# Performance work log

Hardware: AMD Instinct MI355X
Metric: run time of the kernel (lower is better)

## Reference

```python
import jax, jax.numpy as jnp
import numpy as np

NFFT = 640
HOP = 320
REF_CH = 3  # reference microphone index


def _hann(n):
    # periodic Hann, matches torch.hann_window(n)
    return 0.5 * (1.0 - jnp.cos(2.0 * jnp.pi * jnp.arange(n, dtype=jnp.float32) / n))


def _stft(x):
    # x: [..., T] -> complex [..., F, Tf], center=True, constant (zero) pad
    win = _hann(NFFT)
    pad = NFFT // 2
    xp = jnp.pad(x, [(0, 0)] * (x.ndim - 1) + [(pad, pad)])
    T = x.shape[-1]
    nf = 1 + T // HOP
    idx = jnp.arange(nf)[:, None] * HOP + jnp.arange(NFFT)[None, :]
    frames = xp[..., idx] * win  # [..., Tf, NFFT]
    return jnp.swapaxes(jnp.fft.rfft(frames, axis=-1), -1, -2)  # [..., F, Tf]


def _istft(S):
    # S: [..., F, Tf] complex -> real [..., (Tf-1)*HOP]
    win = _hann(NFFT)
    frames = jnp.fft.irfft(jnp.swapaxes(S, -1, -2), n=NFFT, axis=-1) * win
    Tf = S.shape[-1]
    L = (Tf - 1) * HOP + NFFT
    idx = jnp.arange(Tf)[:, None] * HOP + jnp.arange(NFFT)[None, :]
    out = jnp.zeros(S.shape[:-2] + (L,), frames.dtype).at[..., idx].add(frames)
    wsum = jnp.zeros((L,), frames.dtype).at[idx].add(win * win)
    out = out / jnp.where(wsum > 1e-11, wsum, 1.0)
    p = NFFT // 2
    return out[..., p:L - p]


def _cov_features(xb):
    # xb: [C, T] -> [C*(C+1) + 2, F, Tf]
    S = _stft(xb)  # [C, F, Tf] complex
    C = xb.shape[0]
    iu, ju = np.triu_indices(C)  # upper triangle, row-major (matches torch mask order)
    cov = S[iu] * jnp.conj(S[ju])  # [C*(C+1)/2, F, Tf], cov[i,j] = S_i * conj(S_j)
    nF, nT = S.shape[-2], S.shape[-1]
    cov_ri = jnp.stack([cov.real, cov.imag], axis=1).reshape(-1, nF, nT)  # interleave re/im
    ref = S[REF_CH]
    return jnp.concatenate([cov_ri, ref.real[None], ref.imag[None]], axis=0)


def _forward(x, rtf_g, ref_g):
    B, C, T = x.shape
    feats = jax.vmap(_cov_features)(x)  # [B, 74, F, Tf]
    # STFT of generated reference channel
    refS = _stft(ref_g.reshape(B, -1))  # [B, F, Tf] complex
    nF, nT = refS.shape[-2], refS.shape[-1]
    # deep-filtering: unfold kernel (3,9) with padding (1,4) over (freq, frame)
    rp = jnp.pad(refS, ((0, 0), (1, 1), (4, 4)))
    patches = jnp.stack([rp[:, ki:ki + nF, kj:kj + nT]
                         for ki in range(3) for kj in range(9)], axis=1)  # [B, 27, F, Tf]
    rtf_c = (rtf_g[..., 0] + 1j * rtf_g[..., 1]).reshape(B, C - 1, 27, nF, nT)
    est = jnp.einsum('bmkft,bkft->bmft', rtf_c, patches)  # [B, C-1, F, Tf]
    est_audio = _istft(est.reshape(B * (C - 1), nF, nT)).reshape(B, C - 1, -1)
    valid = min(est_audio.shape[-1], ref_g.shape[-1])
    all_ch = jnp.concatenate([est_audio[:, :REF_CH, :valid],
                              ref_g[..., :valid],
                              est_audio[:, REF_CH:, :valid]], axis=1)  # [B, C, valid]
    return all_ch[0].T, feats


def setup_inputs() -> dict:
    key = jax.random.key(0)
    k1, k2, k3 = jax.random.split(key, 3)
    B, C, T = 2, 8, 96000
    nF, nT = NFFT // 2 + 1, 1 + T // HOP  # 321, 301
    x = jax.random.normal(k1, (B, C, T), dtype=jnp.float32)
    rtf_g = jax.random.normal(k2, (B, C - 1, 3, 9, nF, nT, 2), dtype=jnp.float32) * 0.1
    ref_g = jax.random.normal(k3, (B, 1, T), dtype=jnp.float32)
    return {"x": x, "rtf_g": rtf_g, "ref_g": ref_g}


def reference(x, rtf_g, ref_g):
    return _forward(x, rtf_g, ref_g)
```

## Files before the change

kernel.cpp:

```cpp
#include <hip/hip_runtime.h>
#include <math.h>

#define TLEN 96000
#define NFFT 640
#define HOP  320
#define NF   321
#define NT   301
#define FT   (NF * NT)

#define TWO_PI_F 6.28318530717958647692f

__constant__ int IU[36] = {0,0,0,0,0,0,0,0, 1,1,1,1,1,1,1, 2,2,2,2,2,2,
                           3,3,3,3,3, 4,4,4,4, 5,5,5, 6,6, 7};
__constant__ int JU[36] = {0,1,2,3,4,5,6,7, 1,2,3,4,5,6,7, 2,3,4,5,6,7,
                           3,4,5,6,7, 4,5,6,7, 5,6,7, 6,7, 7};

__global__ __launch_bounds__(192) void k_stft(const float* __restrict__ x,
                                              const float* __restrict__ ref_g,
                                              float2* __restrict__ Sx,
                                              float2* __restrict__ refS) {
    const int f   = blockIdx.x;
    const int s   = blockIdx.y;
    const int tid = threadIdx.x;

    __shared__ __align__(16) float2 ff[320];

    const float* sig = (s < 16) ? (x + (size_t)s * TLEN) : ref_g;
    for (int n = tid; n < 320; n += 192) {
        const int p0 = f * HOP + n - HOP;
        const int p1 = p0 + 320;
        const float c = cosf((TWO_PI_F / NFFT) * (float)n);
        float v0 = (p0 >= 0 && p0 < TLEN) ? sig[p0] : 0.0f;
        float v1 = (p1 < TLEN) ? sig[p1] : 0.0f;
        v0 *= (0.5f - 0.5f * c);
        v1 *= (0.5f + 0.5f * c);
        float2 o; o.x = v0 + v1; o.y = v0 - v1;
        ff[n] = o;
    }
    __syncthreads();

    if (tid < 161) {
        const int ke = 2 * tid;
        const int ko = ke + 1;
        const float we = (TWO_PI_F / NFFT) * (float)ke;
        const float wo = (TWO_PI_F / NFFT) * (float)ko;
        const float c2e = 2.0f * cosf(we);
        const float c2o = 2.0f * cosf(wo);

        float se1 = 0.0f, se2 = 0.0f, so1 = 0.0f, so2 = 0.0f;
#pragma unroll 8
        for (int n = 0; n < 320; ++n) {
            const float2 v = ff[n];
            const float te = fmaf(c2e, se1, v.x - se2); se2 = se1; se1 = te;
            const float to = fmaf(c2o, so1, v.y - so2); so2 = so1; so1 = to;
        }

        float sE, cE; sincosf(we, &sE, &cE);
        float sO, cO; sincosf(wo, &sO, &cO);
        float2 Xe, Xo;
        Xe.x = cE * se1 - se2;
        Xe.y = sE * se1;
        Xo.x = -(cO * so1 - so2);
        Xo.y = -(sO * so1);

        if (s < 16) {
            float2* base = Sx + (size_t)s * FT;
            base[(size_t)ke * NT + f] = Xe;
            if (ko < 320) base[(size_t)ko * NT + f] = Xo;
        } else {
            refS[(size_t)ke * NT + f] = Xe;
            if (ko < 320) refS[(size_t)ko * NT + f] = Xo;
        }
    }
}

__global__ void k_cov(const float2* __restrict__ Sx, float* __restrict__ feats) {
    int idx = blockIdx.x * blockDim.x + threadIdx.x;
    if (idx >= 2 * 37 * FT) return;
    const int kt  = idx % FT;
    const int job = (idx / FT) % 37;
    const int b   = idx / (37 * FT);
    const float2* Sb = Sx + (size_t)b * 8 * FT;
    float* fb = feats + (size_t)b * 74 * FT;
    if (job == 36) {
        const float2 r = Sb[(size_t)3 * FT + kt];
        fb[(size_t)72 * FT + kt] = r.x;
        fb[(size_t)73 * FT + kt] = r.y;
    } else {
        const float2 a = Sb[(size_t)IU[job] * FT + kt];
        const float2 c = Sb[(size_t)JU[job] * FT + kt];
        fb[(size_t)(2 * job)     * FT + kt] = a.x * c.x + a.y * c.y;
        fb[(size_t)(2 * job + 1) * FT + kt] = a.y * c.x - a.x * c.y;
    }
}

__global__ void k_dfilter(const float2* __restrict__ rtf,
                          const float2* __restrict__ refS,
                          float2* __restrict__ est) {
    int idx = blockIdx.x * blockDim.x + threadIdx.x;
    if (idx >= 7 * FT) return;
    const int t = idx % NT;
    const int f = (idx / NT) % NF;
    const int m = idx / FT;
    float er = 0.0f, ei = 0.0f;
#pragma unroll
    for (int ki = 0; ki < 3; ++ki) {
        const int ff = f + ki - 1;
#pragma unroll
        for (int kj = 0; kj < 9; ++kj) {
            const int tt = t + kj - 4;
            float pr = 0.0f, pi = 0.0f;
            if ((unsigned)ff < (unsigned)NF && (unsigned)tt < (unsigned)NT) {
                const float2 p = refS[(size_t)ff * NT + tt];
                pr = p.x; pi = p.y;
            }
            const float2 r = rtf[(size_t)(((m * 3 + ki) * 9 + kj) * NF + f) * NT + t];
            er = fmaf(r.x, pr, er); er = fmaf(-r.y, pi, er);
            ei = fmaf(r.x, pi, ei); ei = fmaf( r.y, pr, ei);
        }
    }
    float2 o; o.x = er; o.y = ei;
    est[idx] = o;
}

__global__ __launch_bounds__(320) void k_iframes(const float2* __restrict__ est,
                                                 float* __restrict__ frames) {
    const int f   = blockIdx.x;
    const int m   = blockIdx.y;
    const int tid = threadIdx.x;
    __shared__ __align__(16) float2 X[322];
    for (int k = tid; k < NF; k += 320)
        X[k] = est[((size_t)m * NF + k) * NT + f];
    if (tid == 0) { float2 z; z.x = 0.0f; z.y = 0.0f; X[321] = z; }
    __syncthreads();

    const int n = tid;
    float sp, cp; sincosf((TWO_PI_F / NFFT) * (float)n, &sp, &cp);
    const float c2p = cp * cp - sp * sp;
    const float s2p = 2.0f * sp * cp;
    const float c2  = 2.0f * c2p;

    float er1 = 0.0f, er2 = 0.0f, ei1 = 0.0f, ei2 = 0.0f;
    float or1 = 0.0f, or2 = 0.0f, oi1 = 0.0f, oi2 = 0.0f;
    const float4* Xp = (const float4*)X;
#pragma unroll 4
    for (int j = 0; j < 160; ++j) {
        const float4 v = Xp[j];
        const float t0 = fmaf(c2, er1, v.x - er2); er2 = er1; er1 = t0;
        const float t1 = fmaf(c2, ei1, v.y - ei2); ei2 = ei1; ei1 = t1;
        const float t2 = fmaf(c2, or1, v.z - or2); or2 = or1; or1 = t2;
        const float t3 = fmaf(c2, oi1, v.w - oi2); oi2 = oi1; oi1 = t3;
    }
    {
        const float4 v = Xp[160];
        const float t0 = fmaf(c2, er1, v.x - er2); er2 = er1; er1 = t0;
        const float t1 = fmaf(c2, ei1, v.y - ei2); ei2 = ei1; ei1 = t1;
    }

    const float PEbr = c2p * er1 + s2p * ei1 - er2;
    const float PEbi = c2p * ei1 - s2p * er1 - ei2;
    const float PObr = c2p * or1 + s2p * oi1 - or2;
    const float PObi = c2p * oi1 - s2p * or1 - oi2;

    float sr, crr; sincosf((TWO_PI_F / 320.0f) * (float)n, &sr, &crr);
    const float sgn  = (n & 1) ? -1.0f : 1.0f;
    const float RePE = sgn * (crr * PEbr - sr * PEbi);
    const float RePO = sgn * (cp * PObr - sp * PObi);

    const float base = X[0].x + sgn * X[320].x;
    const float y1 = 2.0f * (RePE + RePO) - base;
    const float y2 = 2.0f * (RePE - RePO) - base;

    const float w0 = 0.5f - 0.5f * cp;
    const float w1 = 0.5f + 0.5f * cp;
    const float inv = 1.0f / NFFT;
    float* fb = frames + ((size_t)m * NT + f) * NFFT;
    fb[n]       = y1 * inv * w0;
    fb[n + 320] = y2 * inv * w1;
}

__global__ void k_ola(const float* __restrict__ frames,
                      const float* __restrict__ ref_g,
                      float* __restrict__ out0) {
    int idx = blockIdx.x * blockDim.x + threadIdx.x;
    if (idx >= 8 * TLEN) return;
    const int c = idx & 7;
    const int t = idx >> 3;
    float o;
    if (c == 3) {
        o = ref_g[t];
    } else {
        const int m  = (c < 3) ? c : (c - 1);
        const int f1 = t / HOP + 1;
        const int n1 = t % HOP;
        const float a = frames[((size_t)m * NT + f1)     * NFFT + n1];
        const float b = frames[((size_t)m * NT + f1 - 1) * NFFT + n1 + 320];
        const float cw = cosf((TWO_PI_F / NFFT) * (float)n1);
        const float w0 = 0.5f - 0.5f * cw;
        const float w1 = 0.5f + 0.5f * cw;
        float ws = w0 * w0 + w1 * w1;
        ws = (ws > 1e-11f) ? ws : 1.0f;
        o = (a + b) / ws;
    }
    out0[idx] = o;
}

extern "C" void kernel_launch(void* const* d_in, const int* in_sizes, int n_in,
                              void* d_out, int out_size, void* d_ws, size_t ws_size,
                              hipStream_t stream) {
    const float* x     = (const float*)d_in[0];
    const float* rtf   = (const float*)d_in[1];
    const float* ref_g = (const float*)d_in[2];

    float* out0  = (float*)d_out;
    float* feats = (float*)d_out + (size_t)8 * TLEN;

    float2* Sx     = (float2*)d_ws;
    float2* refS   = Sx + (size_t)16 * FT;
    float2* est    = refS + (size_t)FT;
    float*  frames = (float*)(est + (size_t)7 * FT);

    k_stft<<<dim3(NT, 17), 192, 0, stream>>>(x, ref_g, Sx, refS);
    {
        const int total = 2 * 37 * FT;
        k_cov<<<(total + 255) / 256, 256, 0, stream>>>(Sx, feats);
    }
    {
        const int total = 7 * FT;
        k_dfilter<<<(total + 255) / 256, 256, 0, stream>>>(
            (const float2*)rtf, refS, est);
    }
    k_iframes<<<dim3(NT, 7), 320, 0, stream>>>(est, frames);
    {
        const int total = 8 * TLEN;
        k_ola<<<(total + 255) / 256, 256, 0, stream>>>(frames, ref_g, out0);
    }
}
```

Before: 457.7 us.

## Compute multichannel STFT as bf16 MFMA DFT matmul and fuse covariance per bin

Replaces the per-frame Goertzel STFT of the 16 microphone signals with a folded even/odd real DFT expressed as a bf16 matrix multiply on MFMA units. Twiddle and framed-signal matrices are built in separate kernels. The covariance kernel now loads all 8 channels for one (batch, bin, frame) once and emits every upper-triangle product, instead of re-reading the spectra per pair. The reference-signal STFT keeps the float path. Using bf16 inputs lowers STFT precision, which risks tolerance failures on the features.

```diff
diff --git a/kernel.cpp b/kernel.cpp
--- a/kernel.cpp
+++ b/kernel.cpp
@@ -8,32 +8,132 @@
 #define NT   301
 #define FT   (NF * NT)
 
+#define NCOL  4816
+#define NCOLP 4864
+#define CSTR  4864
+#define CROWS 656
+
 #define TWO_PI_F 6.28318530717958647692f
 
-__constant__ int IU[36] = {0,0,0,0,0,0,0,0, 1,1,1,1,1,1,1, 2,2,2,2,2,2,
-                           3,3,3,3,3, 4,4,4,4, 5,5,5, 6,6, 7};
-__constant__ int JU[36] = {0,1,2,3,4,5,6,7, 1,2,3,4,5,6,7, 2,3,4,5,6,7,
-                           3,4,5,6,7, 4,5,6,7, 5,6,7, 6,7, 7};
-
-__global__ __launch_bounds__(192) void k_stft(const float* __restrict__ x,
-                                              const float* __restrict__ ref_g,
-                                              float2* __restrict__ Sx,
-                                              float2* __restrict__ refS) {
+typedef __attribute__((ext_vector_type(8))) short bfrag;
+typedef __attribute__((ext_vector_type(4))) float f32x4;
+
+__device__ inline short f2bf(float x) {
+    unsigned u = __float_as_uint(x);
+    u += 0x7fffu + ((u >> 16) & 1u);
+    return (short)(u >> 16);
+}
+
+__global__ __launch_bounds__(320) void k_fold(const float* __restrict__ x,
+                                              short* __restrict__ FEt,
+                                              short* __restrict__ FOt) {
+    const int c = blockIdx.x;
+    const int n = threadIdx.x;
+    short e = 0, o = 0;
+    if (c < NCOL) {
+        const int s = c / NT;
+        const int f = c % NT;
+        const float* sig = x + (size_t)s * TLEN;
+        const int p0 = f * HOP + n - HOP;
+        const int p1 = p0 + HOP;
+        const float cw = cosf((TWO_PI_F / NFFT) * (float)n);
+        float v0 = (p0 >= 0) ? sig[p0] : 0.0f;
+        float v1 = (p1 < TLEN) ? sig[p1] : 0.0f;
+        v0 *= (0.5f - 0.5f * cw);
+        v1 *= (0.5f + 0.5f * cw);
+        e = f2bf(v0 + v1);
+        o = f2bf(v0 - v1);
+    }
+    FEt[(size_t)c * 320 + n] = e;
+    FOt[(size_t)c * 320 + n] = o;
+}
+
+__global__ __launch_bounds__(320) void k_twid(short* __restrict__ Ae,
+                                              short* __restrict__ Ao) {
+    const int m = blockIdx.x;
+    const int n = threadIdx.x;
+    float val = 0.0f;
+    if (m < 336) {
+        if (m < 161) {
+            const int r = (m * n) % 320;
+            val = cosf((TWO_PI_F / 320.0f) * (float)r);
+        } else if (m < 322) {
+            const int r = ((m - 161) * n) % 320;
+            val = -sinf((TWO_PI_F / 320.0f) * (float)r);
+        }
+        Ae[(size_t)m * 320 + n] = f2bf(val);
+    } else {
+        const int mm = m - 336;
+        if (mm < 160) {
+            const int r = ((2 * mm + 1) * n) % 640;
+            val = cosf((TWO_PI_F / 640.0f) * (float)r);
+        } else if (mm < 320) {
+            const int r = ((2 * (mm - 160) + 1) * n) % 640;
+            val = -sinf((TWO_PI_F / 640.0f) * (float)r);
+        }
+        Ao[(size_t)mm * 320 + n] = f2bf(val);
+    }
+}
+
+__global__ __launch_bounds__(256) void k_dftmm(const short* __restrict__ Ae,
+                                               const short* __restrict__ Ao,
+                                               const short* __restrict__ FEt,
+                                               const short* __restrict__ FOt,
+                                               float* __restrict__ C) {
+    const int nt = blockIdx.x;
+    const int mt = blockIdx.y;
+    const bool isE = (mt < 21);
+    const int m0 = (isE ? mt : mt - 21) * 16;
+    const short* A = isE ? Ae : Ao;
+    const short* B = isE ? FEt : FOt;
+    const int crow0 = isE ? 0 : 336;
+
+    const int wave = threadIdx.x >> 6;
+    const int lane = threadIdx.x & 63;
+    const int q    = lane & 15;
+    const int quad = lane >> 4;
+    const int cbase = nt * 256 + wave * 64;
+
+    const short* Arow = A + (size_t)(m0 + q) * 320 + quad * 8;
+    const short* Brow = B + (size_t)(cbase + q) * 320 + quad * 8;
+
+    f32x4 acc0 = {0.f,0.f,0.f,0.f}, acc1 = acc0, acc2 = acc0, acc3 = acc0;
+#pragma unroll
+    for (int kk = 0; kk < 320; kk += 32) {
+        const bfrag a  = *(const bfrag*)(Arow + kk);
+        const bfrag b0 = *(const bfrag*)(Brow + kk);
+        const bfrag b1 = *(const bfrag*)(Brow + (size_t)16 * 320 + kk);
+        const bfrag b2 = *(const bfrag*)(Brow + (size_t)32 * 320 + kk);
+        const bfrag b3 = *(const bfrag*)(Brow + (size_t)48 * 320 + kk);
+        acc0 = __builtin_amdgcn_mfma_f32_16x16x32_bf16(a, b0, acc0, 0, 0, 0);
+        acc1 = __builtin_amdgcn_mfma_f32_16x16x32_bf16(a, b1, acc1, 0, 0, 0);
+        acc2 = __builtin_amdgcn_mfma_f32_16x16x32_bf16(a, b2, acc2, 0, 0, 0);
+        acc3 = __builtin_amdgcn_mfma_f32_16x16x32_bf16(a, b3, acc3, 0, 0, 0);
+    }
+    float* Cb = C + (size_t)(crow0 + m0 + quad * 4) * CSTR + cbase + q;
+#pragma unroll
+    for (int r = 0; r < 4; ++r) {
+        Cb[(size_t)r * CSTR +  0] = acc0[r];
+        Cb[(size_t)r * CSTR + 16] = acc1[r];
+        Cb[(size_t)r * CSTR + 32] = acc2[r];
+        Cb[(size_t)r * CSTR + 48] = acc3[r];
+    }
+}
+
+__global__ __launch_bounds__(192) void k_stft_ref(const float* __restrict__ ref_g,
+                                                  float2* __restrict__ refS) {
     const int f   = blockIdx.x;
-    const int s   = blockIdx.y;
     const int tid = threadIdx.x;
 
     __shared__ __align__(16) float2 ff[320];
-
-    const float* sig = (s < 16) ? (x + (size_t)s * TLEN) : ref_g;
     for (int n = tid; n < 320; n += 192) {
         const int p0 = f * HOP + n - HOP;
-        const int p1 = p0 + 320;
-        const float c = cosf((TWO_PI_F / NFFT) * (float)n);
-        float v0 = (p0 >= 0 && p0 < TLEN) ? sig[p0] : 0.0f;
-        float v1 = (p1 < TLEN) ? sig[p1] : 0.0f;
-        v0 *= (0.5f - 0.5f * c);
-        v1 *= (0.5f + 0.5f * c);
+        const int p1 = p0 + HOP;
+        const float cw = cosf((TWO_PI_F / NFFT) * (float)n);
+        float v0 = (p0 >= 0) ? ref_g[p0] : 0.0f;
+        float v1 = (p1 < TLEN) ? ref_g[p1] : 0.0f;
+        v0 *= (0.5f - 0.5f * cw);
+        v1 *= (0.5f + 0.5f * cw);
         float2 o; o.x = v0 + v1; o.y = v0 - v1;
         ff[n] = o;
     }
@@ -46,7 +146,6 @@
         const float wo = (TWO_PI_F / NFFT) * (float)ko;
         const float c2e = 2.0f * cosf(we);
         const float c2o = 2.0f * cosf(wo);
-
         float se1 = 0.0f, se2 = 0.0f, so1 = 0.0f, so2 = 0.0f;
 #pragma unroll 8
         for (int n = 0; n < 320; ++n) {
@@ -54,44 +153,47 @@
             const float te = fmaf(c2e, se1, v.x - se2); se2 = se1; se1 = te;
             const float to = fmaf(c2o, so1, v.y - so2); so2 = so1; so1 = to;
         }
-
         float sE, cE; sincosf(we, &sE, &cE);
         float sO, cO; sincosf(wo, &sO, &cO);
         float2 Xe, Xo;
-        Xe.x = cE * se1 - se2;
-        Xe.y = sE * se1;
-        Xo.x = -(cO * so1 - so2);
-        Xo.y = -(sO * so1);
-
-        if (s < 16) {
-            float2* base = Sx + (size_t)s * FT;
-            base[(size_t)ke * NT + f] = Xe;
-            if (ko < 320) base[(size_t)ko * NT + f] = Xo;
-        } else {
-            refS[(size_t)ke * NT + f] = Xe;
-            if (ko < 320) refS[(size_t)ko * NT + f] = Xo;
-        }
-    }
-}
-
-__global__ void k_cov(const float2* __restrict__ Sx, float* __restrict__ feats) {
-    int idx = blockIdx.x * blockDim.x + threadIdx.x;
-    if (idx >= 2 * 37 * FT) return;
-    const int kt  = idx % FT;
-    const int job = (idx / FT) % 37;
-    const int b   = idx / (37 * FT);
-    const float2* Sb = Sx + (size_t)b * 8 * FT;
-    float* fb = feats + (size_t)b * 74 * FT;
-    if (job == 36) {
-        const float2 r = Sb[(size_t)3 * FT + kt];
-        fb[(size_t)72 * FT + kt] = r.x;
-        fb[(size_t)73 * FT + kt] = r.y;
-    } else {
-        const float2 a = Sb[(size_t)IU[job] * FT + kt];
-        const float2 c = Sb[(size_t)JU[job] * FT + kt];
-        fb[(size_t)(2 * job)     * FT + kt] = a.x * c.x + a.y * c.y;
-        fb[(size_t)(2 * job + 1) * FT + kt] = a.y * c.x - a.x * c.y;
-    }
+        Xe.x = cE * se1 - se2;   Xe.y = sE * se1;
+        Xo.x = -(cO * so1 - so2); Xo.y = -(sO * so1);
+        refS[(size_t)ke * NT + f] = Xe;
+        if (ko < 320) refS[(size_t)ko * NT + f] = Xo;
+    }
+}
+
+__global__ __launch_bounds__(64) void k_cov(const float* __restrict__ C,
+                                            float* __restrict__ feats) {
+    const int t = blockIdx.x * 64 + threadIdx.x;
+    if (t >= NT) return;
+    const int bk = blockIdx.y;
+    const int b = bk / NF;
+    const int k = bk % NF;
+    const int h = k >> 1;
+    const int m_re = (k & 1) ? 336 + h : h;
+    const int m_im = (k & 1) ? 496 + h : 161 + h;
+    const float* rr = C + (size_t)m_re * CSTR + b * 8 * NT + t;
+    const float* ri = C + (size_t)m_im * CSTR + b * 8 * NT + t;
+    float ar[8], ai[8];
+#pragma unroll
+    for (int s = 0; s < 8; ++s) {
+        ar[s] = rr[s * NT];
+        ai[s] = ri[s * NT];
+    }
+    float* fb = feats + (size_t)b * 74 * FT + (size_t)k * NT + t;
+    int p = 0;
+#pragma unroll
+    for (int i = 0; i < 8; ++i) {
+#pragma unroll
+        for (int j = i; j < 8; ++j) {
+            fb[(size_t)(2 * p)     * FT] = ar[i] * ar[j] + ai[i] * ai[j];
+            fb[(size_t)(2 * p + 1) * FT] = ai[i] * ar[j] - ar[i] * ai[j];
+            ++p;
+        }
+    }
+    fb[(size_t)72 * FT] = ar[3];
+    fb[(size_t)73 * FT] = ai[3];
 }
 
 __global__ void k_dfilter(const float2* __restrict__ rtf,
@@ -156,7 +258,6 @@
         const float t0 = fmaf(c2, er1, v.x - er2); er2 = er1; er1 = t0;
         const float t1 = fmaf(c2, ei1, v.y - ei2); ei2 = ei1; ei1 = t1;
     }
-
     const float PEbr = c2p * er1 + s2p * ei1 - er2;
     const float PEbi = c2p * ei1 - s2p * er1 - ei2;
     const float PObr = c2p * or1 + s2p * oi1 - or2;
@@ -215,16 +316,26 @@
     float* out0  = (float*)d_out;
     float* feats = (float*)d_out + (size_t)8 * TLEN;
 
-    float2* Sx     = (float2*)d_ws;
-    float2* refS   = Sx + (size_t)16 * FT;
-    float2* est    = refS + (size_t)FT;
-    float*  frames = (float*)(est + (size_t)7 * FT);
-
-    k_stft<<<dim3(NT, 17), 192, 0, stream>>>(x, ref_g, Sx, refS);
-    {
-        const int total = 2 * 37 * FT;
-        k_cov<<<(total + 255) / 256, 256, 0, stream>>>(Sx, feats);
-    }
+    char* w = (char*)d_ws;
+    auto carve = [&](size_t bytes) {
+        char* p = w;
+        w += (bytes + 63) & ~(size_t)63;
+        return p;
+    };
+    float*  Cm     = (float*)carve((size_t)CROWS * CSTR * 4);
+    short*  FEt    = (short*)carve((size_t)NCOLP * 320 * 2);
+    short*  FOt    = (short*)carve((size_t)NCOLP * 320 * 2);
+    short*  Ae     = (short*)carve((size_t)336 * 320 * 2);
+    short*  Ao     = (short*)carve((size_t)336 * 320 * 2);
+    float2* refS   = (float2*)carve((size_t)FT * 8);
+    float2* est    = (float2*)carve((size_t)7 * FT * 8);
+    float*  frames = (float*)carve((size_t)7 * NT * NFFT * 4);
+
+    k_fold<<<NCOLP, 320, 0, stream>>>(x, FEt, FOt);
+    k_twid<<<672, 320, 0, stream>>>(Ae, Ao);
+    k_stft_ref<<<NT, 192, 0, stream>>>(ref_g, refS);
+    k_dftmm<<<dim3(19, 41), 256, 0, stream>>>(Ae, Ao, FEt, FOt, Cm);
+    k_cov<<<dim3(5, 2 * NF), 64, 0, stream>>>(Cm, feats);
     {
         const int total = 7 * FT;
         k_dfilter<<<(total + 255) / 256, 256, 0, stream>>>(
```

Measured after the change: 459.7 us. No clear change (+0.4%).
